# Optimization experiments

Measured on AMD Instinct MI355X. Metric: run time of the kernel, lower is better.

Reference implementation:

```python
import jax, jax.numpy as jnp
import numpy as np

B, COND, C, H, W, D = 2, 4, 128, 32, 32, 32
NH = 8            # attention heads
DH = C // NH      # head dim = 16
GROUPS = 8        # GroupNorm groups
EPS = 1e-5


def setup_inputs() -> dict:
    key = jax.random.key(0)
    ks = jax.random.split(key, 12)
    s = 1.0 / np.sqrt(C)
    return {
        "skip_connection_features": jax.random.normal(ks[0], (B, COND, C, H, W, D), jnp.float32),
        "decoder_features": jax.random.normal(ks[1], (B, C, H, W, D), jnp.float32),
        # nn.MultiheadAttention in_proj (split into q/k/v) and out_proj
        "w_q": jax.random.normal(ks[2], (C, C), jnp.float32) * s,
        "w_k": jax.random.normal(ks[3], (C, C), jnp.float32) * s,
        "w_v": jax.random.normal(ks[4], (C, C), jnp.float32) * s,
        "b_q": jnp.zeros((C,), jnp.float32),
        "b_k": jnp.zeros((C,), jnp.float32),
        "b_v": jnp.zeros((C,), jnp.float32),
        "w_o": jax.random.normal(ks[5], (C, C), jnp.float32) * s,
        "b_o": jnp.zeros((C,), jnp.float32),
        # GroupNorm affine params
        "gn_gamma": jnp.ones((C,), jnp.float32),
        "gn_beta": jnp.zeros((C,), jnp.float32),
    }


def reference(skip_connection_features, decoder_features,
              w_q, w_k, w_v, b_q, b_k, b_v, w_o, b_o, gn_gamma, gn_beta):
    # Query: one per voxel. x: [B, H, W, D, C]
    x = jnp.transpose(decoder_features, (0, 2, 3, 4, 1))
    # Keys/values: Cond frames per voxel. y: [B, H, W, D, Cond, C]
    y = jnp.transpose(skip_connection_features, (0, 3, 4, 5, 1, 2))

    q = (x @ w_q.T + b_q).reshape(B, H, W, D, NH, DH)
    k = (y @ w_k.T + b_k).reshape(B, H, W, D, COND, NH, DH)
    v = (y @ w_v.T + b_v).reshape(B, H, W, D, COND, NH, DH)

    # scores: [B, H, W, D, nh, Cond]; scale by 1/sqrt(head_dim) as in torch MHA
    scores = jnp.einsum('bxyzhd,bxyzkhd->bxyzhk', q, k) / np.sqrt(DH)
    attn = jax.nn.softmax(scores, axis=-1)
    o = jnp.einsum('bxyzhk,bxyzkhd->bxyzhd', attn, v).reshape(B, H, W, D, C)
    o = o @ w_o.T + b_o

    # back to channels-first and residual add: [B, C, H, W, D]
    out = jnp.transpose(o, (0, 4, 1, 2, 3)) + decoder_features

    # GroupNorm(8, C) over (group channels, H, W, D)
    g = out.reshape(B, GROUPS, C // GROUPS, H, W, D)
    mu = g.mean(axis=(2, 3, 4, 5), keepdims=True)
    var = g.var(axis=(2, 3, 4, 5), keepdims=True)
    g = ((g - mu) / jnp.sqrt(var + EPS)).reshape(B, C, H, W, D)
    return g * gn_gamma[None, :, None, None, None] + gn_beta[None, :, None, None, None]
```

## Files before the change

kernel.cpp:

```cpp
#include <hip/hip_runtime.h>

#define B_    2
#define COND_ 4
#define C_    128
#define S_    32768
#define NH_   8
#define TS_   64

#define GEMM_Q(SRC, ACC)                                                      \
  _Pragma("unroll 4")                                                         \
  for (int c4 = 0; c4 < 32; ++c4) {                                           \
    const float4 w0_ = *(const float4*)&wbuf[(g << 2) + 0][c4 << 2];          \
    const float4 w1_ = *(const float4*)&wbuf[(g << 2) + 1][c4 << 2];          \
    const float4 w2_ = *(const float4*)&wbuf[(g << 2) + 2][c4 << 2];          \
    const float4 w3_ = *(const float4*)&wbuf[(g << 2) + 3][c4 << 2];          \
    const float2 x0_ = *(const float2*)&SRC[(c4 << 2) + 0][st << 1];          \
    const float2 x1_ = *(const float2*)&SRC[(c4 << 2) + 1][st << 1];          \
    const float2 x2_ = *(const float2*)&SRC[(c4 << 2) + 2][st << 1];          \
    const float2 x3_ = *(const float2*)&SRC[(c4 << 2) + 3][st << 1];          \
    ACC[0][0] += w0_.x * x0_.x + w0_.y * x1_.x + w0_.z * x2_.x + w0_.w * x3_.x; \
    ACC[0][1] += w0_.x * x0_.y + w0_.y * x1_.y + w0_.z * x2_.y + w0_.w * x3_.y; \
    ACC[1][0] += w1_.x * x0_.x + w1_.y * x1_.x + w1_.z * x2_.x + w1_.w * x3_.x; \
    ACC[1][1] += w1_.x * x0_.y + w1_.y * x1_.y + w1_.z * x2_.y + w1_.w * x3_.y; \
    ACC[2][0] += w2_.x * x0_.x + w2_.y * x1_.x + w2_.z * x2_.x + w2_.w * x3_.x; \
    ACC[2][1] += w2_.x * x0_.y + w2_.y * x1_.y + w2_.z * x2_.y + w2_.w * x3_.y; \
    ACC[3][0] += w3_.x * x0_.x + w3_.y * x1_.x + w3_.z * x2_.x + w3_.w * x3_.x; \
    ACC[3][1] += w3_.x * x0_.y + w3_.y * x1_.y + w3_.z * x2_.y + w3_.w * x3_.y; \
  }

__global__ __launch_bounds__(256, 2) void attn_kernel(
    const float* __restrict__ skip,
    const float* __restrict__ dec,
    const float* __restrict__ wq, const float* __restrict__ wk,
    const float* __restrict__ wv,
    const float* __restrict__ bq, const float* __restrict__ bk,
    const float* __restrict__ bv,
    const float* __restrict__ wo, const float* __restrict__ bo,
    float* __restrict__ attn_out,
    float* __restrict__ stats)
{
  __shared__ float sx[C_][TS_];
  __shared__ float sy[C_][TS_];
  __shared__ float wbuf[32][128];

  const int tid = threadIdx.x;
  const int g  = tid >> 5;
  const int st = tid & 31;
  const int b  = blockIdx.y;
  const int s0 = blockIdx.x * TS_;

  {
    const float* base = dec + (size_t)b * C_ * S_ + s0;
    #pragma unroll
    for (int i = 0; i < 8; ++i) {
      int l = i * 256 + tid;
      int c = l >> 4, ss4 = l & 15;
      *(float4*)&sx[c][ss4 * 4] = *(const float4*)(base + (size_t)c * S_ + ss4 * 4);
    }
  }

  #define LOADW(W, QQ)                                                        \
    _Pragma("unroll")                                                         \
    for (int i = 0; i < 4; ++i) {                                             \
      int l = i * 256 + tid;                             \
      int lr = l >> 5, cq = l & 31;                                           \
      int r = (lr >> 2) * 16 + (QQ) * 4 + (lr & 3);                           \
      *(float4*)&wbuf[lr][cq * 4] = *(const float4*)((W) + r * 128 + cq * 4); \
    }

  float qv[16][2];
  float sc[COND_][2];
  #pragma unroll
  for (int c = 0; c < COND_; ++c) { sc[c][0] = 0.f; sc[c][1] = 0.f; }

  for (int qq = 0; qq < 4; ++qq) {
    __syncthreads();
    LOADW(wq, qq);
    __syncthreads();
    float acc[4][2];
    #pragma unroll
    for (int j = 0; j < 4; ++j) {
      float bb = bq[g * 16 + qq * 4 + j];
      acc[j][0] = bb; acc[j][1] = bb;
    }
    GEMM_Q(sx, acc);
    #pragma unroll
    for (int j = 0; j < 4; ++j) {
      qv[qq * 4 + j][0] = acc[j][0];
      qv[qq * 4 + j][1] = acc[j][1];
    }
  }

  for (int cond = 0; cond < COND_; ++cond) {
    __syncthreads();
    {
      const float* ybase = skip + ((size_t)b * COND_ + cond) * C_ * S_ + s0;
      #pragma unroll
      for (int i = 0; i < 8; ++i) {
        int l = i * 256 + tid;
        int c = l >> 4, ss4 = l & 15;
        *(float4*)&sy[c][ss4 * 4] = *(const float4*)(ybase + (size_t)c * S_ + ss4 * 4);
      }
    }
    for (int qq = 0; qq < 4; ++qq) {
      __syncthreads();
      LOADW(wk, qq);
      __syncthreads();
      float acc[4][2];
      #pragma unroll
      for (int j = 0; j < 4; ++j) {
        float bb = bk[g * 16 + qq * 4 + j];
        acc[j][0] = bb; acc[j][1] = bb;
      }
      GEMM_Q(sy, acc);
      #pragma unroll
      for (int j = 0; j < 4; ++j) {
        sc[cond][0] += qv[qq * 4 + j][0] * acc[j][0];
        sc[cond][1] += qv[qq * 4 + j][1] * acc[j][1];
      }
    }
  }

  float attnw[COND_][2];
  #pragma unroll
  for (int ss = 0; ss < 2; ++ss) {
    float m = -1e30f;
    #pragma unroll
    for (int c = 0; c < COND_; ++c) m = fmaxf(m, sc[c][ss] * 0.25f);
    float sum = 0.f, e[COND_];
    #pragma unroll
    for (int c = 0; c < COND_; ++c) { e[c] = expf(sc[c][ss] * 0.25f - m); sum += e[c]; }
    float inv = 1.f / sum;
    #pragma unroll
    for (int c = 0; c < COND_; ++c) attnw[c][ss] = e[c] * inv;
  }

  float ov[16][2];
  #pragma unroll
  for (int i = 0; i < 16; ++i) {
    float bb = bv[g * 16 + i];
    ov[i][0] = bb; ov[i][1] = bb;
  }
  for (int cond = 0; cond < COND_; ++cond) {
    __syncthreads();
    {
      const float* ybase = skip + ((size_t)b * COND_ + cond) * C_ * S_ + s0;
      #pragma unroll
      for (int i = 0; i < 8; ++i) {
        int l = i * 256 + tid;
        int c = l >> 4, ss4 = l & 15;
        *(float4*)&sy[c][ss4 * 4] = *(const float4*)(ybase + (size_t)c * S_ + ss4 * 4);
      }
    }
    for (int qq = 0; qq < 4; ++qq) {
      __syncthreads();
      LOADW(wv, qq);
      __syncthreads();
      float acc[4][2] = {{0.f,0.f},{0.f,0.f},{0.f,0.f},{0.f,0.f}};
      GEMM_Q(sy, acc);
      #pragma unroll
      for (int j = 0; j < 4; ++j) {
        ov[qq * 4 + j][0] += attnw[cond][0] * acc[j][0];
        ov[qq * 4 + j][1] += attnw[cond][1] * acc[j][1];
      }
    }
  }

  __syncthreads();
  #pragma unroll
  for (int i = 0; i < 16; ++i)
    *(float2*)&sy[g * 16 + i][st << 1] = make_float2(ov[i][0], ov[i][1]);

  float gsum = 0.f, gsq = 0.f;
  float* obase = attn_out + (size_t)b * C_ * S_ + s0;
  for (int qq = 0; qq < 4; ++qq) {
    __syncthreads();
    LOADW(wo, qq);
    __syncthreads();
    float acc[4][2];
    #pragma unroll
    for (int j = 0; j < 4; ++j) {
      float bb = bo[g * 16 + qq * 4 + j];
      acc[j][0] = bb; acc[j][1] = bb;
    }
    GEMM_Q(sy, acc);
    #pragma unroll
    for (int j = 0; j < 4; ++j) {
      int r = g * 16 + qq * 4 + j;
      float o0 = acc[j][0] + sx[r][(st << 1) + 0];
      float o1 = acc[j][1] + sx[r][(st << 1) + 1];
      *(float2*)(obase + (size_t)r * S_ + (st << 1)) = make_float2(o0, o1);
      gsum += o0 + o1;
      gsq  += o0 * o0 + o1 * o1;
    }
  }

  #pragma unroll
  for (int off = 16; off >= 1; off >>= 1) {
    gsum += __shfl_xor(gsum, off, 32);
    gsq  += __shfl_xor(gsq,  off, 32);
  }
  if (st == 0) {
    atomicAdd(&stats[(b * 8 + g) * 2 + 0], gsum);
    atomicAdd(&stats[(b * 8 + g) * 2 + 1], gsq);
  }
}

__global__ void gn_kernel(const float* __restrict__ src, const float* __restrict__ stats,
                          const float* __restrict__ gamma, const float* __restrict__ beta,
                          float* __restrict__ out)
{
  const int n4 = B_ * C_ * S_ / 4;
  const float inv_n = 1.0f / (16.0f * S_);
  int i = blockIdx.x * blockDim.x + threadIdx.x;
  for (; i < n4; i += gridDim.x * blockDim.x) {
    int bc = i >> 13;
    int b = bc >> 7, c = bc & 127;
    int gi = (b * 8 + (c >> 4)) * 2;
    float mu  = stats[gi] * inv_n;
    float var = stats[gi + 1] * inv_n - mu * mu;
    float rs  = rsqrtf(var + 1e-5f);
    float ga  = gamma[c] * rs;
    float be  = beta[c] - mu * ga;
    float4 v = ((const float4*)src)[i];
    float4 o;
    o.x = v.x * ga + be; o.y = v.y * ga + be;
    o.z = v.z * ga + be; o.w = v.w * ga + be;
    ((float4*)out)[i] = o;
  }
}

extern "C" void kernel_launch(void* const* d_in, const int* in_sizes, int n_in,
                              void* d_out, int out_size, void* d_ws, size_t ws_size,
                              hipStream_t stream) {
  const float* skip  = (const float*)d_in[0];
  const float* dec   = (const float*)d_in[1];
  const float* wq    = (const float*)d_in[2];
  const float* wk    = (const float*)d_in[3];
  const float* wv    = (const float*)d_in[4];
  const float* bq    = (const float*)d_in[5];
  const float* bk    = (const float*)d_in[6];
  const float* bv    = (const float*)d_in[7];
  const float* wo    = (const float*)d_in[8];
  const float* bo    = (const float*)d_in[9];
  const float* gamma = (const float*)d_in[10];
  const float* beta  = (const float*)d_in[11];

  float* out     = (float*)d_out;
  float* ws_attn = (float*)d_ws;
  float* stats   = ws_attn + (size_t)B_ * C_ * S_;

  hipMemsetAsync(stats, 0, 32 * sizeof(float), stream);

  dim3 grid(S_ / TS_, B_);
  attn_kernel<<<grid, 256, 0, stream>>>(skip, dec, wq, wk, wv, bq, bk, bv, wo, bo,
                                        ws_attn, stats);
  gn_kernel<<<2048, 256, 0, stream>>>(ws_attn, stats, gamma, beta, out);
}
```

Before: 649.4 us.

## Rewrite attention kernel on fp16 split-precision MFMA with fp16 intermediate

Replaces the scalar fp32 GEMM attention kernel with a 64-thread-per-block kernel that runs the Q/K/V/O projections as 16x16x32 fp16 MFMA. Precision is kept close to fp32 by splitting each operand into hi and lo fp16 parts and issuing three products per step. A separate kernel converts the weights once per call into hi/lo fp16 buffers that are read straight from global memory. The intermediate attention output is stored as fp16 to halve GroupNorm read traffic, which costs some accuracy. The new block is much smaller and does per-lane strided global stores, so occupancy and coalescing patterns change.

```diff
diff --git a/kernel.cpp b/kernel.cpp
--- a/kernel.cpp
+++ b/kernel.cpp
@@ -4,229 +4,273 @@
 #define COND_ 4
 #define C_    128
 #define S_    32768
-#define NH_   8
-#define TS_   64
-
-#define GEMM_Q(SRC, ACC)                                                      \
-  _Pragma("unroll 4")                                                         \
-  for (int c4 = 0; c4 < 32; ++c4) {                                           \
-    const float4 w0_ = *(const float4*)&wbuf[(g << 2) + 0][c4 << 2];          \
-    const float4 w1_ = *(const float4*)&wbuf[(g << 2) + 1][c4 << 2];          \
-    const float4 w2_ = *(const float4*)&wbuf[(g << 2) + 2][c4 << 2];          \
-    const float4 w3_ = *(const float4*)&wbuf[(g << 2) + 3][c4 << 2];          \
-    const float2 x0_ = *(const float2*)&SRC[(c4 << 2) + 0][st << 1];          \
-    const float2 x1_ = *(const float2*)&SRC[(c4 << 2) + 1][st << 1];          \
-    const float2 x2_ = *(const float2*)&SRC[(c4 << 2) + 2][st << 1];          \
-    const float2 x3_ = *(const float2*)&SRC[(c4 << 2) + 3][st << 1];          \
-    ACC[0][0] += w0_.x * x0_.x + w0_.y * x1_.x + w0_.z * x2_.x + w0_.w * x3_.x; \
-    ACC[0][1] += w0_.x * x0_.y + w0_.y * x1_.y + w0_.z * x2_.y + w0_.w * x3_.y; \
-    ACC[1][0] += w1_.x * x0_.x + w1_.y * x1_.x + w1_.z * x2_.x + w1_.w * x3_.x; \
-    ACC[1][1] += w1_.x * x0_.y + w1_.y * x1_.y + w1_.z * x2_.y + w1_.w * x3_.y; \
-    ACC[2][0] += w2_.x * x0_.x + w2_.y * x1_.x + w2_.z * x2_.x + w2_.w * x3_.x; \
-    ACC[2][1] += w2_.x * x0_.y + w2_.y * x1_.y + w2_.z * x2_.y + w2_.w * x3_.y; \
-    ACC[3][0] += w3_.x * x0_.x + w3_.y * x1_.x + w3_.z * x2_.x + w3_.w * x3_.x; \
-    ACC[3][1] += w3_.x * x0_.y + w3_.y * x1_.y + w3_.z * x2_.y + w3_.w * x3_.y; \
-  }
-
-__global__ __launch_bounds__(256, 2) void attn_kernel(
-    const float* __restrict__ skip,
-    const float* __restrict__ dec,
-    const float* __restrict__ wq, const float* __restrict__ wk,
-    const float* __restrict__ wv,
+#define VT_   16
+#define LDT_  136
+
+typedef __attribute__((ext_vector_type(8))) _Float16 f16x8;
+typedef __attribute__((ext_vector_type(4))) _Float16 f16x4;
+typedef __attribute__((ext_vector_type(4))) float    f32x4;
+
+#define MFMA16(a,b,c) __builtin_amdgcn_mfma_f32_16x16x32_f16((a),(b),(c),0,0,0)
+
+__device__ __forceinline__ void stage_tile_hl(const float* __restrict__ g,
+                                              _Float16* __restrict__ Th,
+                                              _Float16* __restrict__ Tl, int t) {
+  const int vq  = t & 3;
+  const int ch0 = (t >> 2) * 8;
+  f32x4 f[8];
+  #pragma unroll
+  for (int r = 0; r < 8; ++r)
+    f[r] = *(const f32x4*)(g + (size_t)(ch0 + r) * S_ + vq * 4);
+  #pragma unroll
+  for (int i = 0; i < 4; ++i) {
+    f16x8 hh, ll;
+    #pragma unroll
+    for (int r = 0; r < 8; ++r) {
+      float x = f[r][i];
+      _Float16 h = (_Float16)x;
+      hh[r] = h;
+      ll[r] = (_Float16)(x - (float)h);
+    }
+    const int v = vq * 4 + i;
+    *(f16x8*)&Th[v * LDT_ + ch0] = hh;
+    *(f16x8*)&Tl[v * LDT_ + ch0] = ll;
+  }
+}
+
+__global__ void wcvt_kernel(const float* __restrict__ wq, const float* __restrict__ wk,
+                            const float* __restrict__ wv, const float* __restrict__ wo,
+                            _Float16* __restrict__ Wh, _Float16* __restrict__ Wl) {
+  int i = blockIdx.x * 256 + threadIdx.x;
+  const float* src[4] = {wq, wk, wv, wo};
+  #pragma unroll
+  for (int m = 0; m < 4; ++m) {
+    float x = src[m][i];
+    _Float16 h = (_Float16)x;
+    Wh[m * 16384 + i] = h;
+    Wl[m * 16384 + i] = (_Float16)(x - (float)h);
+  }
+}
+
+__global__ __launch_bounds__(64) void attn_kernel(
+    const float* __restrict__ skip, const float* __restrict__ dec,
+    const _Float16* __restrict__ Wh, const _Float16* __restrict__ Wl,
     const float* __restrict__ bq, const float* __restrict__ bk,
-    const float* __restrict__ bv,
-    const float* __restrict__ wo, const float* __restrict__ bo,
-    float* __restrict__ attn_out,
-    float* __restrict__ stats)
-{
-  __shared__ float sx[C_][TS_];
-  __shared__ float sy[C_][TS_];
-  __shared__ float wbuf[32][128];
-
-  const int tid = threadIdx.x;
-  const int g  = tid >> 5;
-  const int st = tid & 31;
-  const int b  = blockIdx.y;
-  const int s0 = blockIdx.x * TS_;
-
-  {
-    const float* base = dec + (size_t)b * C_ * S_ + s0;
-    #pragma unroll
-    for (int i = 0; i < 8; ++i) {
-      int l = i * 256 + tid;
-      int c = l >> 4, ss4 = l & 15;
-      *(float4*)&sx[c][ss4 * 4] = *(const float4*)(base + (size_t)c * S_ + ss4 * 4);
-    }
-  }
-
-  #define LOADW(W, QQ)                                                        \
-    _Pragma("unroll")                                                         \
-    for (int i = 0; i < 4; ++i) {                                             \
-      int l = i * 256 + tid;                             \
-      int lr = l >> 5, cq = l & 31;                                           \
-      int r = (lr >> 2) * 16 + (QQ) * 4 + (lr & 3);                           \
-      *(float4*)&wbuf[lr][cq * 4] = *(const float4*)((W) + r * 128 + cq * 4); \
-    }
-
-  float qv[16][2];
-  float sc[COND_][2];
-  #pragma unroll
-  for (int c = 0; c < COND_; ++c) { sc[c][0] = 0.f; sc[c][1] = 0.f; }
-
-  for (int qq = 0; qq < 4; ++qq) {
-    __syncthreads();
-    LOADW(wq, qq);
-    __syncthreads();
-    float acc[4][2];
-    #pragma unroll
-    for (int j = 0; j < 4; ++j) {
-      float bb = bq[g * 16 + qq * 4 + j];
-      acc[j][0] = bb; acc[j][1] = bb;
-    }
-    GEMM_Q(sx, acc);
-    #pragma unroll
-    for (int j = 0; j < 4; ++j) {
-      qv[qq * 4 + j][0] = acc[j][0];
-      qv[qq * 4 + j][1] = acc[j][1];
-    }
-  }
-
-  for (int cond = 0; cond < COND_; ++cond) {
-    __syncthreads();
-    {
-      const float* ybase = skip + ((size_t)b * COND_ + cond) * C_ * S_ + s0;
+    const float* __restrict__ bv, const float* __restrict__ bo,
+    _Float16* __restrict__ ws_attn, float* __restrict__ stats) {
+  __shared__ _Float16 skh[COND_][VT_ * LDT_];
+  __shared__ _Float16 skl[COND_][VT_ * LDT_];
+  __shared__ _Float16 sxh[VT_ * LDT_];
+  __shared__ _Float16 sxl[VT_ * LDT_];
+  __shared__ _Float16 so[VT_ * LDT_];
+
+  const int l   = threadIdx.x;
+  const int b   = blockIdx.y;
+  const int s0  = blockIdx.x * VT_;
+  const int row = l & 15;
+  const int kh  = l >> 4;
+  const int vox = row;
+
+  stage_tile_hl(dec + (size_t)b * C_ * S_ + s0, sxh, sxl, l);
+  #pragma unroll
+  for (int c = 0; c < COND_; ++c)
+    stage_tile_hl(skip + ((size_t)(b * COND_ + c)) * C_ * S_ + s0, skh[c], skl[c], l);
+  __syncthreads();
+
+  f32x4 q[8];
+  f16x8 bxh[4], bxl[4];
+  #pragma unroll
+  for (int ks = 0; ks < 4; ++ks) {
+    bxh[ks] = *(const f16x8*)&sxh[vox * LDT_ + ks * 32 + kh * 8];
+    bxl[ks] = *(const f16x8*)&sxl[vox * LDT_ + ks * 32 + kh * 8];
+  }
+  #pragma unroll
+  for (int m = 0; m < 8; ++m) {
+    f16x8 ah[4], al[4];
+    #pragma unroll
+    for (int ks = 0; ks < 4; ++ks) {
+      const size_t off = (size_t)(m * 16 + row) * 128 + ks * 32 + kh * 8;
+      ah[ks] = *(const f16x8*)(Wh + off);
+      al[ks] = *(const f16x8*)(Wl + off);
+    }
+    f32x4 acc = *(const f32x4*)(bq + m * 16 + kh * 4);
+    #pragma unroll
+    for (int ks = 0; ks < 4; ++ks) {
+      acc = MFMA16(al[ks], bxh[ks], acc);
+      acc = MFMA16(ah[ks], bxl[ks], acc);
+      acc = MFMA16(ah[ks], bxh[ks], acc);
+    }
+    q[m] = acc;
+  }
+
+  float sc[8][4];
+  #pragma unroll
+  for (int m = 0; m < 8; ++m) {
+    f16x8 ah[4], al[4];
+    #pragma unroll
+    for (int ks = 0; ks < 4; ++ks) {
+      const size_t off = 16384 + (size_t)(m * 16 + row) * 128 + ks * 32 + kh * 8;
+      ah[ks] = *(const f16x8*)(Wh + off);
+      al[ks] = *(const f16x8*)(Wl + off);
+    }
+    #pragma unroll
+    for (int c = 0; c < COND_; ++c) {
+      f16x8 bh[4], bl[4];
       #pragma unroll
-      for (int i = 0; i < 8; ++i) {
-        int l = i * 256 + tid;
-        int c = l >> 4, ss4 = l & 15;
-        *(float4*)&sy[c][ss4 * 4] = *(const float4*)(ybase + (size_t)c * S_ + ss4 * 4);
+      for (int ks = 0; ks < 4; ++ks) {
+        bh[ks] = *(const f16x8*)&skh[c][vox * LDT_ + ks * 32 + kh * 8];
+        bl[ks] = *(const f16x8*)&skl[c][vox * LDT_ + ks * 32 + kh * 8];
       }
-    }
-    for (int qq = 0; qq < 4; ++qq) {
-      __syncthreads();
-      LOADW(wk, qq);
-      __syncthreads();
-      float acc[4][2];
+      f32x4 acc = *(const f32x4*)(bk + m * 16 + kh * 4);
       #pragma unroll
-      for (int j = 0; j < 4; ++j) {
-        float bb = bk[g * 16 + qq * 4 + j];
-        acc[j][0] = bb; acc[j][1] = bb;
+      for (int ks = 0; ks < 4; ++ks) {
+        acc = MFMA16(al[ks], bh[ks], acc);
+        acc = MFMA16(ah[ks], bl[ks], acc);
+        acc = MFMA16(ah[ks], bh[ks], acc);
       }
-      GEMM_Q(sy, acc);
+      float p = q[m].x * acc.x + q[m].y * acc.y + q[m].z * acc.z + q[m].w * acc.w;
+      p += __shfl_xor(p, 16);
+      p += __shfl_xor(p, 32);
+      sc[m][c] = p;
+    }
+  }
+
+  float attw[8][4];
+  #pragma unroll
+  for (int m = 0; m < 8; ++m) {
+    float t0 = sc[m][0] * 0.25f, t1 = sc[m][1] * 0.25f;
+    float t2 = sc[m][2] * 0.25f, t3 = sc[m][3] * 0.25f;
+    float mx = fmaxf(fmaxf(t0, t1), fmaxf(t2, t3));
+    float e0 = expf(t0 - mx), e1 = expf(t1 - mx);
+    float e2 = expf(t2 - mx), e3 = expf(t3 - mx);
+    float inv = 1.0f / (e0 + e1 + e2 + e3);
+    attw[m][0] = e0 * inv; attw[m][1] = e1 * inv;
+    attw[m][2] = e2 * inv; attw[m][3] = e3 * inv;
+  }
+
+  f32x4 o[8];
+  #pragma unroll
+  for (int m = 0; m < 8; ++m) o[m] = *(const f32x4*)(bv + m * 16 + kh * 4);
+  #pragma unroll
+  for (int m = 0; m < 8; ++m) {
+    f16x8 ah[4], al[4];
+    #pragma unroll
+    for (int ks = 0; ks < 4; ++ks) {
+      const size_t off = 32768 + (size_t)(m * 16 + row) * 128 + ks * 32 + kh * 8;
+      ah[ks] = *(const f16x8*)(Wh + off);
+      al[ks] = *(const f16x8*)(Wl + off);
+    }
+    #pragma unroll
+    for (int c = 0; c < COND_; ++c) {
+      f16x8 bh[4], bl[4];
       #pragma unroll
-      for (int j = 0; j < 4; ++j) {
-        sc[cond][0] += qv[qq * 4 + j][0] * acc[j][0];
-        sc[cond][1] += qv[qq * 4 + j][1] * acc[j][1];
+      for (int ks = 0; ks < 4; ++ks) {
+        bh[ks] = *(const f16x8*)&skh[c][vox * LDT_ + ks * 32 + kh * 8];
+        bl[ks] = *(const f16x8*)&skl[c][vox * LDT_ + ks * 32 + kh * 8];
       }
-    }
-  }
-
-  float attnw[COND_][2];
-  #pragma unroll
-  for (int ss = 0; ss < 2; ++ss) {
-    float m = -1e30f;
-    #pragma unroll
-    for (int c = 0; c < COND_; ++c) m = fmaxf(m, sc[c][ss] * 0.25f);
-    float sum = 0.f, e[COND_];
-    #pragma unroll
-    for (int c = 0; c < COND_; ++c) { e[c] = expf(sc[c][ss] * 0.25f - m); sum += e[c]; }
-    float inv = 1.f / sum;
-    #pragma unroll
-    for (int c = 0; c < COND_; ++c) attnw[c][ss] = e[c] * inv;
-  }
-
-  float ov[16][2];
-  #pragma unroll
-  for (int i = 0; i < 16; ++i) {
-    float bb = bv[g * 16 + i];
-    ov[i][0] = bb; ov[i][1] = bb;
-  }
-  for (int cond = 0; cond < COND_; ++cond) {
-    __syncthreads();
-    {
-      const float* ybase = skip + ((size_t)b * COND_ + cond) * C_ * S_ + s0;
+      f32x4 acc = {0.f, 0.f, 0.f, 0.f};
       #pragma unroll
-      for (int i = 0; i < 8; ++i) {
-        int l = i * 256 + tid;
-        int c = l >> 4, ss4 = l & 15;
-        *(float4*)&sy[c][ss4 * 4] = *(const float4*)(ybase + (size_t)c * S_ + ss4 * 4);
+      for (int ks = 0; ks < 4; ++ks) {
+        acc = MFMA16(al[ks], bh[ks], acc);
+        acc = MFMA16(ah[ks], bl[ks], acc);
+        acc = MFMA16(ah[ks], bh[ks], acc);
       }
-    }
-    for (int qq = 0; qq < 4; ++qq) {
-      __syncthreads();
-      LOADW(wv, qq);
-      __syncthreads();
-      float acc[4][2] = {{0.f,0.f},{0.f,0.f},{0.f,0.f},{0.f,0.f}};
-      GEMM_Q(sy, acc);
-      #pragma unroll
-      for (int j = 0; j < 4; ++j) {
-        ov[qq * 4 + j][0] += attnw[cond][0] * acc[j][0];
-        ov[qq * 4 + j][1] += attnw[cond][1] * acc[j][1];
-      }
-    }
-  }
-
+      const float w = attw[m][c];
+      o[m].x += w * acc.x; o[m].y += w * acc.y;
+      o[m].z += w * acc.z; o[m].w += w * acc.w;
+    }
+  }
+
+  #pragma unroll
+  for (int m = 0; m < 8; ++m) {
+    f16x4 h;
+    h[0] = (_Float16)o[m].x; h[1] = (_Float16)o[m].y;
+    h[2] = (_Float16)o[m].z; h[3] = (_Float16)o[m].w;
+    *(f16x4*)&so[vox * LDT_ + m * 16 + kh * 4] = h;
+  }
   __syncthreads();
-  #pragma unroll
-  for (int i = 0; i < 16; ++i)
-    *(float2*)&sy[g * 16 + i][st << 1] = make_float2(ov[i][0], ov[i][1]);
-
-  float gsum = 0.f, gsq = 0.f;
-  float* obase = attn_out + (size_t)b * C_ * S_ + s0;
-  for (int qq = 0; qq < 4; ++qq) {
-    __syncthreads();
-    LOADW(wo, qq);
-    __syncthreads();
-    float acc[4][2];
-    #pragma unroll
-    for (int j = 0; j < 4; ++j) {
-      float bb = bo[g * 16 + qq * 4 + j];
-      acc[j][0] = bb; acc[j][1] = bb;
-    }
-    GEMM_Q(sy, acc);
-    #pragma unroll
-    for (int j = 0; j < 4; ++j) {
-      int r = g * 16 + qq * 4 + j;
-      float o0 = acc[j][0] + sx[r][(st << 1) + 0];
-      float o1 = acc[j][1] + sx[r][(st << 1) + 1];
-      *(float2*)(obase + (size_t)r * S_ + (st << 1)) = make_float2(o0, o1);
-      gsum += o0 + o1;
-      gsq  += o0 * o0 + o1 * o1;
-    }
-  }
-
-  #pragma unroll
-  for (int off = 16; off >= 1; off >>= 1) {
-    gsum += __shfl_xor(gsum, off, 32);
-    gsq  += __shfl_xor(gsq,  off, 32);
-  }
-  if (st == 0) {
-    atomicAdd(&stats[(b * 8 + g) * 2 + 0], gsum);
-    atomicAdd(&stats[(b * 8 + g) * 2 + 1], gsq);
-  }
-}
-
-__global__ void gn_kernel(const float* __restrict__ src, const float* __restrict__ stats,
+
+  f16x8 b8[4];
+  #pragma unroll
+  for (int ks = 0; ks < 4; ++ks)
+    b8[ks] = *(const f16x8*)&so[vox * LDT_ + ks * 32 + kh * 8];
+
+  float gsm[8], gsq[8];
+  const float* dbase = dec + (size_t)b * C_ * S_ + s0 + vox;
+  _Float16* obase = ws_attn + (size_t)b * C_ * S_ + s0 + vox;
+  #pragma unroll
+  for (int m = 0; m < 8; ++m) {
+    f16x8 ah[4], al[4];
+    #pragma unroll
+    for (int ks = 0; ks < 4; ++ks) {
+      const size_t off = 49152 + (size_t)(m * 16 + row) * 128 + ks * 32 + kh * 8;
+      ah[ks] = *(const f16x8*)(Wh + off);
+      al[ks] = *(const f16x8*)(Wl + off);
+    }
+    f32x4 acc = *(const f32x4*)(bo + m * 16 + kh * 4);
+    #pragma unroll
+    for (int ks = 0; ks < 4; ++ks) {
+      acc = MFMA16(al[ks], b8[ks], acc);
+      acc = MFMA16(ah[ks], b8[ks], acc);
+    }
+    const int ch = m * 16 + kh * 4;
+    acc.x += dbase[(size_t)(ch + 0) * S_];
+    acc.y += dbase[(size_t)(ch + 1) * S_];
+    acc.z += dbase[(size_t)(ch + 2) * S_];
+    acc.w += dbase[(size_t)(ch + 3) * S_];
+    _Float16 h0 = (_Float16)acc.x, h1 = (_Float16)acc.y;
+    _Float16 h2 = (_Float16)acc.z, h3 = (_Float16)acc.w;
+    obase[(size_t)(ch + 0) * S_] = h0;
+    obase[(size_t)(ch + 1) * S_] = h1;
+    obase[(size_t)(ch + 2) * S_] = h2;
+    obase[(size_t)(ch + 3) * S_] = h3;
+    float f0 = (float)h0, f1 = (float)h1, f2 = (float)h2, f3 = (float)h3;
+    gsm[m] = f0 + f1 + f2 + f3;
+    gsq[m] = f0 * f0 + f1 * f1 + f2 * f2 + f3 * f3;
+  }
+
+  #pragma unroll
+  for (int m = 0; m < 8; ++m) {
+    float s1 = gsm[m], s2 = gsq[m];
+    #pragma unroll
+    for (int off = 32; off >= 1; off >>= 1) {
+      s1 += __shfl_xor(s1, off);
+      s2 += __shfl_xor(s2, off);
+    }
+    gsm[m] = s1; gsq[m] = s2;
+  }
+  if (l == 0) {
+    #pragma unroll
+    for (int m = 0; m < 8; ++m) {
+      atomicAdd(&stats[(b * 8 + m) * 2 + 0], gsm[m]);
+      atomicAdd(&stats[(b * 8 + m) * 2 + 1], gsq[m]);
+    }
+  }
+}
+
+__global__ void gn_kernel(const _Float16* __restrict__ src, const float* __restrict__ stats,
                           const float* __restrict__ gamma, const float* __restrict__ beta,
-                          float* __restrict__ out)
-{
-  const int n4 = B_ * C_ * S_ / 4;
+                          float* __restrict__ out) {
+  const int n8 = B_ * C_ * S_ / 8;
   const float inv_n = 1.0f / (16.0f * S_);
-  int i = blockIdx.x * blockDim.x + threadIdx.x;
-  for (; i < n4; i += gridDim.x * blockDim.x) {
-    int bc = i >> 13;
-    int b = bc >> 7, c = bc & 127;
+  for (int i = blockIdx.x * blockDim.x + threadIdx.x; i < n8; i += gridDim.x * blockDim.x) {
+    int e0 = i << 3;
+    int bc = e0 >> 15;
+    int c = bc & 127, b = bc >> 7;
     int gi = (b * 8 + (c >> 4)) * 2;
     float mu  = stats[gi] * inv_n;
     float var = stats[gi + 1] * inv_n - mu * mu;
     float rs  = rsqrtf(var + 1e-5f);
     float ga  = gamma[c] * rs;
     float be  = beta[c] - mu * ga;
-    float4 v = ((const float4*)src)[i];
-    float4 o;
-    o.x = v.x * ga + be; o.y = v.y * ga + be;
-    o.z = v.z * ga + be; o.w = v.w * ga + be;
-    ((float4*)out)[i] = o;
+    f16x8 v = *(const f16x8*)(src + e0);
+    float4 o0, o1;
+    o0.x = (float)v[0] * ga + be; o0.y = (float)v[1] * ga + be;
+    o0.z = (float)v[2] * ga + be; o0.w = (float)v[3] * ga + be;
+    o1.x = (float)v[4] * ga + be; o1.y = (float)v[5] * ga + be;
+    o1.z = (float)v[6] * ga + be; o1.w = (float)v[7] * ga + be;
+    *(float4*)(out + e0)     = o0;
+    *(float4*)(out + e0 + 4) = o1;
   }
 }
 
@@ -246,14 +290,14 @@
   const float* gamma = (const float*)d_in[10];
   const float* beta  = (const float*)d_in[11];
 
-  float* out     = (float*)d_out;
-  float* ws_attn = (float*)d_ws;
-  float* stats   = ws_attn + (size_t)B_ * C_ * S_;
+  _Float16* Wh    = (_Float16*)d_ws;
+  _Float16* Wl    = (_Float16*)((char*)d_ws + 131072);
+  float*    stats = (float*)((char*)d_ws + 262144);
+  _Float16* ws_at = (_Float16*)((char*)d_ws + 262272);
 
   hipMemsetAsync(stats, 0, 32 * sizeof(float), stream);
-
-  dim3 grid(S_ / TS_, B_);
-  attn_kernel<<<grid, 256, 0, stream>>>(skip, dec, wq, wk, wv, bq, bk, bv, wo, bo,
-                                        ws_attn, stats);
-  gn_kernel<<<2048, 256, 0, stream>>>(ws_attn, stats, gamma, beta, out);
-}
+  wcvt_kernel<<<64, 256, 0, stream>>>(wq, wk, wv, wo, Wh, Wl);
+  attn_kernel<<<dim3(S_ / VT_, B_), 64, 0, stream>>>(skip, dec, Wh, Wl, bq, bk, bv, bo,
+                                                     ws_at, stats);
+  gn_kernel<<<2048, 256, 0, stream>>>(ws_at, stats, gamma, beta, (float*)d_out);
+}
```

Result: slower. 1.015 ms (+56.2%).
